# Optimization experiments

Measured on AMD Instinct MI355X. Metric: run time of the kernel, lower is better.

Reference implementation:

```python
import jax, jax.numpy as jnp
import numpy as np

B, M, L = 100, 100, 8
N = M * L
EPS = 1e-5  # torch BatchNorm2d default eps


def _conv(x, w, b, stride, pad):
    y = jax.lax.conv_general_dilated(x, w, (stride, stride), [(pad, pad), (pad, pad)],
                                     dimension_numbers=('NCHW', 'OIHW', 'NCHW'))
    return y + b[None, :, None, None]


def _convT(x, w, b, stride, pad):
    # torch ConvTranspose2d weight layout: (in_ch, out_ch, kH, kW)
    k = w.shape[2]
    wt = jnp.flip(w, (2, 3)).transpose(1, 0, 2, 3)  # -> OIHW
    p = k - 1 - pad
    y = jax.lax.conv_general_dilated(x, wt, (1, 1), [(p, p), (p, p)],
                                     lhs_dilation=(stride, stride),
                                     dimension_numbers=('NCHW', 'OIHW', 'NCHW'))
    return y + b[None, :, None, None]


def _bn(x):
    # BatchNorm2d constructed fresh in forward: weight=1, bias=0, batch stats (biased var)
    mean = x.mean(axis=(0, 2, 3), keepdims=True)
    var = x.var(axis=(0, 2, 3), keepdims=True)
    return (x - mean) / jnp.sqrt(var + EPS)


def _leaky(x):
    return jnp.where(x >= 0, x, 0.01 * x)


def _forward(x, conv1_w, conv1_b, conv2_w, conv2_b, conv3_w, conv3_b, conv4_w, conv4_b,
             fc_w, fc_b, dec_w, dec_b, ct1_w, ct1_b, ct2_w, ct2_b, ct3_w, ct3_b,
             ct4_w, ct4_b, ct5_w, ct5_b):
    # ---- encoder ----
    h = _bn(_leaky(_conv(x, conv1_w, conv1_b, 2, 1)))   # (B,128,32,32)
    h = _bn(_leaky(_conv(h, conv2_w, conv2_b, 2, 1)))   # (B,256,16,16)
    h = _bn(_leaky(_conv(h, conv3_w, conv3_b, 2, 1)))   # (B,1024,8,8)
    h = _bn(_leaky(_conv(h, conv4_w, conv4_b, 2, 1)))   # (B,1024,4,4)
    eig = jax.nn.relu(h.reshape(B, -1) @ fc_w + fc_b)   # (B, 800)
    # ---- latent_sample (training branch) ----
    sig = eig.reshape(B, M, L)
    row = jnp.sqrt(float(M * L)) * jnp.fft.ifft2(sig)          # complex (B,M,L)
    # original builds C via numpy/scipy per-sample -> detached; circulant[i,j] = c[(i-j) % n]
    row_flat = jax.lax.stop_gradient(row.real.reshape(B, N))
    i = jnp.arange(N)
    idx = (i[:, None] - i[None, :]) % N                        # (N,N) circulant gather
    C = row_flat[:, idx]                                       # (B,N,N)
    # original: Sigma_batch_eps[:, i] = eigenvalue (noise zeta is dead code), via numpy -> detached
    Y = jnp.fft.fft2(jax.lax.stop_gradient(sig)).real          # (B,M,L)
    # ---- decoder ----
    d = (Y.reshape(B, N) @ dec_w + dec_b).reshape(B, 1024, 3, 3)
    d = _convT(d, ct1_w, ct1_b, 2, 1)   # (B,512,5,5)
    d = _convT(d, ct2_w, ct2_b, 2, 0)   # (B,256,11,11)
    d = _convT(d, ct3_w, ct3_b, 2, 0)   # (B,128,23,23)
    d = _convT(d, ct4_w, ct4_b, 2, 0)   # (B,64,47,47)
    d = _convT(d, ct5_w, ct5_b, 1, 0)   # (B,1,49,49)
    return d, C, eig


def setup_inputs():
    key = jax.random.key(0)
    ks = jax.random.split(key, 16)

    def wv(k, shape, fan_in):
        return (jax.random.normal(k, shape, jnp.float32) / np.sqrt(fan_in)).astype(jnp.float32)

    return {
        'x': jax.random.normal(ks[0], (B, 1, 64, 64), jnp.float32),
        'conv1_w': wv(ks[1], (128, 1, 3, 3), 9), 'conv1_b': jnp.zeros((128,), jnp.float32),
        'conv2_w': wv(ks[2], (256, 128, 3, 3), 128 * 9), 'conv2_b': jnp.zeros((256,), jnp.float32),
        'conv3_w': wv(ks[3], (1024, 256, 3, 3), 256 * 9), 'conv3_b': jnp.zeros((1024,), jnp.float32),
        'conv4_w': wv(ks[4], (1024, 1024, 3, 3), 1024 * 9), 'conv4_b': jnp.zeros((1024,), jnp.float32),
        'fc_w': wv(ks[5], (1024 * 16, N), 1024 * 16), 'fc_b': jnp.zeros((N,), jnp.float32),
        'dec_w': wv(ks[6], (N, 1024 * 9), N), 'dec_b': jnp.zeros((1024 * 9,), jnp.float32),
        'ct1_w': wv(ks[7], (1024, 512, 3, 3), 1024 * 9), 'ct1_b': jnp.zeros((512,), jnp.float32),
        'ct2_w': wv(ks[8], (512, 256, 3, 3), 512 * 9), 'ct2_b': jnp.zeros((256,), jnp.float32),
        'ct3_w': wv(ks[9], (256, 128, 3, 3), 256 * 9), 'ct3_b': jnp.zeros((128,), jnp.float32),
        'ct4_w': wv(ks[10], (128, 64, 3, 3), 128 * 9), 'ct4_b': jnp.zeros((64,), jnp.float32),
        'ct5_w': wv(ks[11], (64, 1, 3, 3), 64 * 9), 'ct5_b': jnp.zeros((1,), jnp.float32),
    }


def reference(x, conv1_w, conv1_b, conv2_w, conv2_b, conv3_w, conv3_b, conv4_w, conv4_b,
              fc_w, fc_b, dec_w, dec_b, ct1_w, ct1_b, ct2_w, ct2_b, ct3_w, ct3_b,
              ct4_w, ct4_b, ct5_w, ct5_b):
    return _forward(x, conv1_w, conv1_b, conv2_w, conv2_b, conv3_w, conv3_b, conv4_w, conv4_b,
                    fc_w, fc_b, dec_w, dec_b, ct1_w, ct1_b, ct2_w, ct2_b, ct3_w, ct3_b,
                    ct4_w, ct4_b, ct5_w, ct5_b)
```

## Files before the change

kernel.cpp:

```cpp
#include <hip/hip_runtime.h>
#include <math.h>

typedef __attribute__((ext_vector_type(8))) short bf16x8;
typedef __attribute__((ext_vector_type(4))) float f32x4;
typedef unsigned short u16;

__device__ __forceinline__ u16 f2bf(float f) {
    unsigned u = __builtin_bit_cast(unsigned, f);
    u += 0x7FFFu + ((u >> 16) & 1u);
    return (u16)(u >> 16);
}
__device__ __forceinline__ float bf2f(u16 h) {
    unsigned u = ((unsigned)h) << 16;
    return __builtin_bit_cast(float, u);
}

__device__ __align__(64) unsigned g_zeros[16];

__device__ __forceinline__ void gll16(const u16* g, u16* l) {
    __builtin_amdgcn_global_load_lds(
        (const __attribute__((address_space(1))) unsigned*)g,
        (__attribute__((address_space(3))) unsigned*)l, 16, 0, 0);
}

template<int MODE, int OUT, int BM, int BN, int SWIZ, bool STATS, bool PF>
__global__ __launch_bounds__(256, 3)
void gemm(const u16* __restrict__ Abf, const u16* __restrict__ Bw,
          const float* __restrict__ bias, void* __restrict__ outv,
          float* __restrict__ stat,
          int M, int N, int K, int lgC,
          int IH, int IW, int OH, int OW, int zchunk)
{
    constexpr int ANSEG = BM / 64;
    constexpr int ACALLS = BM / 64;
    constexpr int BCALLS = BN / 64;
    constexpr int RM = BM / 32, RN = BN / 32;
    __shared__ __align__(16) u16 As[BM * 32];
    __shared__ __align__(16) u16 Bs[BN * 32];
    const int t = threadIdx.x;
    const int lane = t & 63, wave = t >> 6;
    const int lm = lane & 15, quad = lane >> 4;
    const int wm = wave & 1, wn = wave >> 1;
    int mt, nt, z;
    if (SWIZ == 1) {
        int mtN = (M + BM - 1) / BM;
        int id = blockIdx.x;
        nt = id & 7; int j = id >> 3;
        mt = j % mtN; z = j / mtN;
    } else { mt = blockIdx.x; nt = blockIdx.y; z = blockIdx.z; }
    const int k0 = z * zchunk, kend = k0 + zchunk;

    const int sl_row  = (wave << 4) + (lane >> 2);
    const int sl_koff = (lane & 3) * 8;

    const u16* bsrc[BCALLS]; int bmask[BCALLS];
    #pragma unroll
    for (int s = 0; s < BCALLS; s++) {
        int rg = nt * BN + s * 64 + sl_row;
        bool ok = rg < N;
        bsrc[s] = ok ? (Bw + (size_t)rg * K + sl_koff)
                     : ((const u16*)g_zeros + sl_koff);
        bmask[s] = ok ? ~0 : 0;
    }

    const u16* asrc[ACALLS]; int amask[ACALLS];
    if constexpr (MODE == 0) {
        #pragma unroll
        for (int s = 0; s < ACALLS; s++) {
            int rg = mt * BM + s * 64 + sl_row;
            bool ok = rg < M;
            asrc[s] = ok ? (Abf + (size_t)rg * K + sl_koff)
                         : ((const u16*)g_zeros + sl_koff);
            amask[s] = ok ? ~0 : 0;
        }
    }
    const int arow = (ANSEG == 2) ? (t >> 1) : (t >> 2);
    const int akb  = (ANSEG == 2) ? (t & 1) * 16 : (t & 3) * 8;
    const int a_gm = mt * BM + arow;
    const bool a_in = a_gm < M;
    int oy = 0, ox = 0, bimg = 0;
    const int Cmask = (1 << lgC) - 1;
    int ic_s = 0, tap_s = 0;
    bool aok = a_in;
    const u16* aptr = Abf;
    if constexpr (MODE == 1) {
        int ohw = OH * OW;
        int g = a_in ? a_gm : 0;
        bimg = g / ohw; int r = g - bimg * ohw;
        oy = r / OW; ox = r - (r / OW) * OW;
        int kk0 = k0 + akb;
        tap_s = kk0 >> lgC; ic_s = kk0 & Cmask;
        int ky = tap_s / 3, kx = tap_s - (tap_s / 3) * 3;
        int iy = oy * 2 - 1 + ky, ix = ox * 2 - 1 + kx;
        aok = a_in && (unsigned)iy < (unsigned)IH && (unsigned)ix < (unsigned)IW;
        aptr = Abf + ((((size_t)bimg * IH + iy) * IW + ix) << lgC);
    }
    auto ldA = [&](uint4 (&v)[ANSEG]) {
        #pragma unroll
        for (int s = 0; s < ANSEG; s++) {
            uint4 x4 = make_uint4(0, 0, 0, 0);
            if (aok) x4 = *(const uint4*)(aptr + ic_s + s * 8);
            v[s] = x4;
        }
        ic_s += 32;
        if (ic_s > Cmask) {
            ic_s -= Cmask + 1;
            tap_s++;
            int ky = tap_s / 3, kx = tap_s - (tap_s / 3) * 3;
            int iy = oy * 2 - 1 + ky, ix = ox * 2 - 1 + kx;
            aok = a_in && (unsigned)iy < (unsigned)IH && (unsigned)ix < (unsigned)IW;
            aptr = Abf + ((((size_t)bimg * IH + iy) * IW + ix) << lgC);
        }
    };

    f32x4 acc[RM][RN];
    #pragma unroll
    for (int i = 0; i < RM; i++)
        #pragma unroll
        for (int j = 0; j < RN; j++) acc[i][j] = (f32x4){0.f, 0.f, 0.f, 0.f};

    uint4 va[ANSEG];
    if (MODE == 1 && PF) ldA(va);
    for (int kb = k0; kb < kend; kb += 32) {
        if constexpr (MODE == 1) {
            if (!PF) ldA(va);
            #pragma unroll
            for (int s = 0; s < ANSEG; s++)
                *(uint4*)&As[(((akb >> 3) + s) * BM + arow) * 8] = va[s];
        } else {
            #pragma unroll
            for (int s = 0; s < ACALLS; s++)
                gll16(asrc[s] + (kb & amask[s]),
                      &As[(size_t)(s * 64 + (wave << 4)) * 32]);
        }
        #pragma unroll
        for (int s = 0; s < BCALLS; s++)
            gll16(bsrc[s] + (kb & bmask[s]),
                  &Bs[(size_t)(s * 64 + (wave << 4)) * 32]);
        __syncthreads();
        if (MODE == 1 && PF && kb + 32 < kend) ldA(va);
        bf16x8 af[RM], bfr[RN];
        #pragma unroll
        for (int i = 0; i < RM; i++) {
            if constexpr (MODE == 0)
                af[i] = *(const bf16x8*)&As[(wm * (BM / 2) + i * 16 + lm) * 32 + quad * 8];
            else
                af[i] = *(const bf16x8*)&As[(size_t)(quad * BM + wm * (BM / 2) + i * 16 + lm) * 8];
        }
        #pragma unroll
        for (int j = 0; j < RN; j++)
            bfr[j] = *(const bf16x8*)&Bs[(wn * (BN / 2) + j * 16 + lm) * 32 + quad * 8];
        #pragma unroll
        for (int i = 0; i < RM; i++)
            #pragma unroll
            for (int j = 0; j < RN; j++)
                acc[i][j] = __builtin_amdgcn_mfma_f32_16x16x32_bf16(af[i], bfr[j], acc[i][j], 0, 0, 0);
        __syncthreads();
    }

    const int n_base = nt * BN + wn * (BN / 2);
    const int m_base = mt * BM + wm * (BM / 2);
    int nj[RN]; float bvj[RN];
    #pragma unroll
    for (int j = 0; j < RN; j++) {
        nj[j] = n_base + j * 16 + lm;
        bvj[j] = 0.f;
        if (nj[j] < N && OUT != 4) {
            if (OUT == 0 || OUT == 5) bvj[j] = bias[nj[j]];
            else if (z == 0) bvj[j] = bias[nj[j]];
        }
    }
    if constexpr (OUT == 4) {
        float* op = (float*)outv;
        #pragma unroll
        for (int i = 0; i < RM; i++)
            #pragma unroll
            for (int r = 0; r < 4; r++) {
                int m = m_base + i * 16 + quad * 4 + r;
                if (m >= M) continue;
                #pragma unroll
                for (int j = 0; j < RN; j++)
                    if (nj[j] < N) atomicAdd(&op[(size_t)m * N + nj[j]], acc[i][j][r]);
            }
    } else if constexpr (OUT == 5) {
        u16* op = (u16*)outv;
        #pragma unroll
        for (int j = 0; j < RN; j++) {
            if (nj[j] >= N) continue;
            int c = nj[j] / 9, hw = nj[j] - c * 9;
            #pragma unroll
            for (int i = 0; i < RM; i++)
                #pragma unroll
                for (int r = 0; r < 4; r++) {
                    int m = m_base + i * 16 + quad * 4 + r;
                    if (m >= M) continue;
                    op[((size_t)m * 9 + hw) * 1024 + c] = f2bf(acc[i][j][r] + bvj[j]);
                }
        }
    } else if constexpr (OUT == 0) {
        int ohw = OH * OW;
        float sj[RN], qj[RN];
        #pragma unroll
        for (int j = 0; j < RN; j++) { sj[j] = 0.f; qj[j] = 0.f; }
        #pragma unroll
        for (int i = 0; i < RM; i++) {
            int m0 = m_base + i * 16 + quad * 4;
            if (m0 >= M) continue;
            int b = m0 / ohw, pix = m0 - b * ohw;
            #pragma unroll
            for (int j = 0; j < RN; j++) {
                if (nj[j] >= N) continue;
                #pragma unroll
                for (int r = 0; r < 4; r++) {
                    float val = acc[i][j][r] + bvj[j];
                    ((u16*)outv)[((size_t)b * ohw + pix + r) * N + nj[j]] = f2bf(val);
                    if (STATS) {
                        float lv = val >= 0.f ? val : 0.01f * val;
                        sj[j] += lv; qj[j] += lv * lv;
                    }
                }
            }
        }
        if constexpr (STATS) {
            #pragma unroll
            for (int j = 0; j < RN; j++) {
                float s = sj[j], q = qj[j];
                s += __shfl_down(s, 32); q += __shfl_down(q, 32);
                s += __shfl_down(s, 16); q += __shfl_down(q, 16);
                if (quad == 0 && nj[j] < N) {
                    atomicAdd(&stat[nj[j]], s);
                    atomicAdd(&stat[N + nj[j]], q);
                }
            }
        }
    } else {
        int ohw = OH * OW;
        #pragma unroll
        for (int i = 0; i < RM; i++) {
            int m0 = m_base + i * 16 + quad * 4;
            if (m0 >= M) continue;
            int b = m0 / ohw, pix = m0 - b * ohw;
            #pragma unroll
            for (int j = 0; j < RN; j++) {
                if (nj[j] >= N) continue;
                #pragma unroll
                for (int r = 0; r < 4; r++)
                    atomicAdd(&((float*)outv)[((size_t)b * ohw + pix + r) * N + nj[j]],
                              acc[i][j][r] + bvj[j]);
            }
        }
    }
}

template<int BM, int BN>
__global__ __launch_bounds__(256, 3)
void gemm_ct(const u16* __restrict__ Abf, const u16* __restrict__ Wb,
             const float* __restrict__ bias, u16* __restrict__ out,
             int N, int lgC, int IH, int IW, int OH, int OW,
             int4 Kc, int4 Mc, int4 Hc, int4 Wc, int4 Oc, int4 Dy, int4 Dx)
{
    constexpr int ANSEG = BM / 64;
    constexpr int BCALLS = BN / 64;
    constexpr int RM = BM / 32, RN = BN / 32;
    const int c = blockIdx.z;
    const int Ks[4] = {Kc.x, Kc.y, Kc.z, Kc.w};
    const int Ms[4] = {Mc.x, Mc.y, Mc.z, Mc.w};
    const int Hs[4] = {Hc.x, Hc.y, Hc.z, Hc.w};
    const int Wsz[4]= {Wc.x, Wc.y, Wc.z, Wc.w};
    const int Os[4] = {Oc.x, Oc.y, Oc.z, Oc.w};
    const int Dys[4]= {Dy.x, Dy.y, Dy.z, Dy.w};
    const int Dxs[4]= {Dx.x, Dx.y, Dx.z, Dx.w};
    const int K = Ks[c], M = Ms[c], OHc = Hs[c], OWc = Wsz[c];
    const int dyp = Dys[c], dxp = Dxs[c];
    const int mt = blockIdx.x, nt = blockIdx.y;
    if (mt * BM >= M) return;
    const u16* Bw = Wb + Os[c];

    __shared__ __align__(16) u16 As[BM * 32];
    __shared__ __align__(16) u16 Bs[BN * 32];
    const int t = threadIdx.x;
    const int lane = t & 63, wave = t >> 6;
    const int lm = lane & 15, quad = lane >> 4;
    const int wm = wave & 1, wn = wave >> 1;

    const int sl_row  = (wave << 4) + (lane >> 2);
    const int sl_koff = (lane & 3) * 8;
    const u16* bsrc[BCALLS];
    #pragma unroll
    for (int s = 0; s < BCALLS; s++) {
        int rg = nt * BN + s * 64 + sl_row;
        bsrc[s] = Bw + (size_t)rg * K + sl_koff;
    }

    const int arow = (ANSEG == 2) ? (t >> 1) : (t >> 2);
    const int akb  = (ANSEG == 2) ? (t & 1) * 16 : (t & 3) * 8;
    const int a_gm = mt * BM + arow;
    const bool a_in = a_gm < M;
    const int ohwc = OHc * OWc;
    int g = a_in ? a_gm : 0;
    int bimg = g / ohwc; int rr = g - bimg * ohwc;
    int oy = rr / OWc, ox = rr - (rr / OWc) * OWc;

    const int Cmask = (1 << lgC) - 1;
    int ic_s = akb & Cmask;
    int ti_s = 0;
    bool aok; const u16* aptr;
    {
        int sh = 8 * (ti_s & 3);
        int dy = (int)(signed char)((dyp >> sh) & 255);
        int dx = (int)(signed char)((dxp >> sh) & 255);
        int iy = oy + dy, ix = ox + dx;
        aok = a_in && (unsigned)iy < (unsigned)IH && (unsigned)ix < (unsigned)IW;
        aptr = Abf + ((((size_t)bimg * IH + iy) * IW + ix) << lgC);
    }
    auto ldA = [&](uint4 (&v)[ANSEG]) {
        #pragma unroll
        for (int s = 0; s < ANSEG; s++) {
            uint4 x4 = make_uint4(0, 0, 0, 0);
            if (aok) x4 = *(const uint4*)(aptr + ic_s + s * 8);
            v[s] = x4;
        }
        ic_s += 32;
        if (ic_s > Cmask) {
            ic_s -= Cmask + 1;
            ti_s++;
            int sh = 8 * (ti_s & 3);
            int dy = (int)(signed char)((dyp >> sh) & 255);
            int dx = (int)(signed char)((dxp >> sh) & 255);
            int iy = oy + dy, ix = ox + dx;
            aok = a_in && (unsigned)iy < (unsigned)IH && (unsigned)ix < (unsigned)IW;
            aptr = Abf + ((((size_t)bimg * IH + iy) * IW + ix) << lgC);
        }
    };

    f32x4 acc[RM][RN];
    #pragma unroll
    for (int i = 0; i < RM; i++)
        #pragma unroll
        for (int j = 0; j < RN; j++) acc[i][j] = (f32x4){0.f, 0.f, 0.f, 0.f};

    uint4 va[ANSEG];
    ldA(va);
    for (int kb = 0; kb < K; kb += 32) {
        #pragma unroll
        for (int s = 0; s < ANSEG; s++)
            *(uint4*)&As[(((akb >> 3) + s) * BM + arow) * 8] = va[s];
        #pragma unroll
        for (int s = 0; s < BCALLS; s++)
            gll16(bsrc[s] + kb, &Bs[(size_t)(s * 64 + (wave << 4)) * 32]);
        __syncthreads();
        if (kb + 32 < K) ldA(va);
        bf16x8 af[RM], bfr[RN];
        #pragma unroll
        for (int i = 0; i < RM; i++)
            af[i] = *(const bf16x8*)&As[(size_t)(quad * BM + wm * (BM / 2) + i * 16 + lm) * 8];
        #pragma unroll
        for (int j = 0; j < RN; j++)
            bfr[j] = *(const bf16x8*)&Bs[(wn * (BN / 2) + j * 16 + lm) * 32 + quad * 8];
        #pragma unroll
        for (int i = 0; i < RM; i++)
            #pragma unroll
            for (int j = 0; j < RN; j++)
                acc[i][j] = __builtin_amdgcn_mfma_f32_16x16x32_bf16(af[i], bfr[j], acc[i][j], 0, 0, 0);
        __syncthreads();
    }

    const int n_base = nt * BN + wn * (BN / 2);
    const int m_base = mt * BM + wm * (BM / 2);
    const int cy = c >> 1, cx = c & 1;
    const int OHW = OH * OW;
    int nj[RN]; float bvj[RN];
    #pragma unroll
    for (int j = 0; j < RN; j++) {
        nj[j] = n_base + j * 16 + lm;
        bvj[j] = (nj[j] < N) ? bias[nj[j]] : 0.f;
    }
    #pragma unroll
    for (int i = 0; i < RM; i++)
        #pragma unroll
        for (int r = 0; r < 4; r++) {
            int m = m_base + i * 16 + quad * 4 + r;
            if (m >= M) continue;
            int b = m / ohwc, r2 = m - b * ohwc;
            int oyc = r2 / OWc, oxc = r2 - (r2 / OWc) * OWc;
            size_t ad0 = ((size_t)b * OHW + (2 * oyc + cy) * OW + 2 * oxc + cx) * N;
            #pragma unroll
            for (int j = 0; j < RN; j++)
                if (nj[j] < N) out[ad0 + nj[j]] = f2bf(acc[i][j][r] + bvj[j]);
        }
}

__global__ __launch_bounds__(256)
void convw_prep(const float* __restrict__ src, u16* __restrict__ dst, int lgC) {
    __shared__ float tl[9216];
    int CIN = 1 << lgC;
    int n = CIN * 9;
    size_t base = (size_t)blockIdx.x * n;
    for (int i = threadIdx.x; i < n; i += 256) tl[i] = src[base + i];
    __syncthreads();
    for (int j = threadIdx.x; j < n; j += 256) {
        int tap = j >> lgC, ic = j & (CIN - 1);
        dst[base + j] = f2bf(tl[ic * 9 + tap]);
    }
}

__global__ __launch_bounds__(256)
void transpose_cvt(const float* __restrict__ in, u16* __restrict__ out, int R, int C) {
    __shared__ float tl[32][33];
    int c0 = blockIdx.x * 32, r0 = blockIdx.y * 32;
    int tx = threadIdx.x & 31, ty = threadIdx.x >> 5;
    #pragma unroll
    for (int l = 0; l < 4; l++)
        tl[ty + 8 * l][tx] = in[(size_t)(r0 + ty + 8 * l) * C + c0 + tx];
    __syncthreads();
    #pragma unroll
    for (int l = 0; l < 4; l++)
        out[(size_t)(c0 + ty + 8 * l) * R + r0 + tx] = f2bf(tl[tx][ty + 8 * l]);
}

__global__ __launch_bounds__(256)
void ctw_fused(const float* __restrict__ in, u16* __restrict__ outw,
               int CIN, int P, int4 Kc, int4 Oc) {
    __shared__ float tl[32][33];
    int c0 = blockIdx.x * 32, r0 = blockIdx.y * 32;
    int C = gridDim.x * 32;
    int tx = threadIdx.x & 31, ty = threadIdx.x >> 5;
    #pragma unroll
    for (int l = 0; l < 4; l++)
        tl[ty + 8 * l][tx] = in[(size_t)(r0 + ty + 8 * l) * C + c0 + tx];
    __syncthreads();
    const int Ks[4] = {Kc.x, Kc.y, Kc.z, Kc.w};
    const int Os[4] = {Oc.x, Oc.y, Oc.z, Oc.w};
    int ic = r0 + tx;
    #pragma unroll
    for (int l = 0; l < 4; l++) {
        int cc = c0 + ty + 8 * l;
        int oc = cc / 9, tap = cc - 9 * oc;
        int ky = tap / 3, kx = tap - 3 * (tap / 3);
        int cyc = (P + ky) & 1, cxc = (P + kx) & 1;
        int cls = cyc * 2 + cxc;
        int nkx = ((P ^ cxc) & 1) ? 1 : 2;
        int ti = (ky >> 1) * nkx + (kx >> 1);
        outw[Os[cls] + (size_t)oc * Ks[cls] + ti * CIN + ic] = f2bf(tl[tx][ty + 8 * l]);
    }
}

__global__ __launch_bounds__(256)
void fcw_prep(const float* __restrict__ in, u16* __restrict__ out) {
    __shared__ float tl[32][33];
    int n0 = blockIdx.x * 32, c0 = blockIdx.y * 32, hw = blockIdx.z;
    int tx = threadIdx.x & 31, ty = threadIdx.x >> 5;
    #pragma unroll
    for (int l = 0; l < 4; l++)
        tl[ty + 8 * l][tx] = in[((size_t)(c0 + ty + 8 * l) * 16 + hw) * 800 + n0 + tx];
    __syncthreads();
    #pragma unroll
    for (int l = 0; l < 4; l++)
        out[(size_t)(n0 + ty + 8 * l) * 16384 + hw * 1024 + c0 + tx] = f2bf(tl[tx][ty + 8 * l]);
}

__global__ __launch_bounds__(256)
void wt5_prep(const float* __restrict__ in, u16* __restrict__ out) {
    int idx = blockIdx.x * 256 + threadIdx.x;
    if (idx >= 576) return;
    int tap = idx >> 6, ic = idx & 63;
    out[idx] = f2bf(in[ic * 9 + tap]);
}

__global__ __launch_bounds__(256)
void conv1_nhwc(const float* __restrict__ x, const float* __restrict__ w,
                const float* __restrict__ bias, u16* __restrict__ out) {
    int idx = blockIdx.x * 256 + threadIdx.x;
    if (idx >= 100 * 1024 * 128) return;
    int oc = idx & 127;
    int pix = (idx >> 7) & 1023;
    int b = idx >> 17;
    int oy = pix >> 5, ox = pix & 31;
    int iy0 = oy * 2 - 1, ix0 = ox * 2 - 1;
    float acc = bias[oc];
    const float* ip = x + (size_t)b * 4096;
    const float* wp = w + oc * 9;
    #pragma unroll
    for (int ky = 0; ky < 3; ky++) {
        int iy = iy0 + ky;
        if ((unsigned)iy >= 64u) continue;
        #pragma unroll
        for (int kx = 0; kx < 3; kx++) {
            int ix = ix0 + kx;
            if ((unsigned)ix >= 64u) continue;
            acc = fmaf(ip[iy * 64 + ix], wp[ky * 3 + kx], acc);
        }
    }
    out[idx] = f2bf(acc);
}

__global__ __launch_bounds__(256)
void bnstat8(const u16* __restrict__ x, float* __restrict__ accum, int C, int total) {
    __shared__ float ls[2048];
    for (int i = threadIdx.x; i < 2 * C; i += 256) ls[i] = 0.f;
    __syncthreads();
    int base = (blockIdx.x * 256 + threadIdx.x) * 8;
    int stride = gridDim.x * 256 * 8;
    float s[8], q[8];
    #pragma unroll
    for (int r = 0; r < 8; r++) { s[r] = 0.f; q[r] = 0.f; }
    for (int i = base; i < total; i += stride) {
        uint4 v = *(const uint4*)(x + i);
        const unsigned* w = (const unsigned*)&v;
        #pragma unroll
        for (int h = 0; h < 4; h++) {
            float v0 = __builtin_bit_cast(float, w[h] << 16);
            float v1 = __builtin_bit_cast(float, w[h] & 0xFFFF0000u);
            v0 = v0 >= 0.f ? v0 : 0.01f * v0;
            v1 = v1 >= 0.f ? v1 : 0.01f * v1;
            s[2 * h] += v0;     q[2 * h] += v0 * v0;
            s[2 * h + 1] += v1; q[2 * h + 1] += v1 * v1;
        }
    }
    int c0 = base & (C - 1);
    #pragma unroll
    for (int r = 0; r < 8; r++) {
        atomicAdd(&ls[c0 + r], s[r]);
        atomicAdd(&ls[C + c0 + r], q[r]);
    }
    __syncthreads();
    for (int i = threadIdx.x; i < 2 * C; i += 256) atomicAdd(&accum[i], ls[i]);
}

__global__ __launch_bounds__(256)
void bnapply8(const u16* __restrict__ x, u16* __restrict__ out,
              const float* __restrict__ accum, int C, int total, float invcnt) {
    int i8 = (blockIdx.x * 256 + threadIdx.x) * 8;
    if (i8 >= total) return;
    int c0 = i8 & (C - 1);
    uint4 v = *(const uint4*)(x + i8);
    const unsigned* w = (const unsigned*)&v;
    uint4 o;
    unsigned* ow = (unsigned*)&o;
    #pragma unroll
    for (int h = 0; h < 4; h++) {
        float m0 = accum[c0 + 2 * h] * invcnt, m1 = accum[c0 + 2 * h + 1] * invcnt;
        float q0 = accum[C + c0 + 2 * h] * invcnt, q1 = accum[C + c0 + 2 * h + 1] * invcnt;
        float in0 = rsqrtf(q0 - m0 * m0 + 1e-5f);
        float in1 = rsqrtf(q1 - m1 * m1 + 1e-5f);
        float v0 = __builtin_bit_cast(float, w[h] << 16);
        float v1 = __builtin_bit_cast(float, w[h] & 0xFFFF0000u);
        v0 = v0 >= 0.f ? v0 : 0.01f * v0;
        v1 = v1 >= 0.f ? v1 : 0.01f * v1;
        unsigned r0 = f2bf((v0 - m0) * in0);
        unsigned r1 = f2bf((v1 - m1) * in1);
        ow[h] = r0 | (r1 << 16);
    }
    *(uint4*)(out + i8) = o;
}

__global__ __launch_bounds__(256)
void bnstat4f(const float* __restrict__ x, float* __restrict__ accum, int C, int total) {
    __shared__ float ls[2048];
    for (int i = threadIdx.x; i < 2 * C; i += 256) ls[i] = 0.f;
    __syncthreads();
    int base = (blockIdx.x * 256 + threadIdx.x) * 4;
    int stride = gridDim.x * 1024;
    float s[4] = {0, 0, 0, 0}, q[4] = {0, 0, 0, 0};
    for (int i = base; i < total; i += stride) {
        f32x4 v = *(const f32x4*)(x + i);
        #pragma unroll
        for (int r = 0; r < 4; r++) {
            float vv = v[r]; vv = vv >= 0.f ? vv : 0.01f * vv;
            s[r] += vv; q[r] += vv * vv;
        }
    }
    int c0 = base & (C - 1);
    #pragma unroll
    for (int r = 0; r < 4; r++) {
        atomicAdd(&ls[c0 + r], s[r]);
        atomicAdd(&ls[C + c0 + r], q[r]);
    }
    __syncthreads();
    for (int i = threadIdx.x; i < 2 * C; i += 256) atomicAdd(&accum[i], ls[i]);
}

__global__ __launch_bounds__(256)
void bnapply4f(const float* __restrict__ x, u16* __restrict__ out,
               const float* __restrict__ accum, int C, int total, float invcnt) {
    int i4 = (blockIdx.x * 256 + threadIdx.x) * 4;
    if (i4 >= total) return;
    int c0 = i4 & (C - 1);
    f32x4 v = *(const f32x4*)(x + i4);
    unsigned r4[4];
    #pragma unroll
    for (int r = 0; r < 4; r++) {
        float m = accum[c0 + r] * invcnt;
        float var = accum[C + c0 + r] * invcnt - m * m;
        float inv = rsqrtf(var + 1e-5f);
        float vv = v[r]; vv = vv >= 0.f ? vv : 0.01f * vv;
        r4[r] = f2bf((vv - m) * inv);
    }
    *(uint2*)(out + i4) = make_uint2(r4[0] | (r4[1] << 16), r4[2] | (r4[3] << 16));
}

__global__ __launch_bounds__(256)
void finalize_relu(const float* __restrict__ acc, const float* __restrict__ bias,
                   float* __restrict__ out) {
    int i = blockIdx.x * 256 + threadIdx.x;
    if (i >= 100 * 800) return;
    float v = acc[i] + bias[i % 800];
    out[i] = fmaxf(v, 0.f);
}

__global__ __launch_bounds__(256)
void dft_real(const float* __restrict__ eig, float* __restrict__ Yr, u16* __restrict__ Yrb) {
    __shared__ float se[800];
    __shared__ float ctab[800];
    int b = blockIdx.x;
    for (int i = threadIdx.x; i < 800; i += 256) {
        se[i] = eig[b * 800 + i];
        ctab[i] = cospif(i * 0.0025f);
    }
    __syncthreads();
    int o0 = blockIdx.y * 400;
    for (int oi = o0 + threadIdx.x; oi < o0 + 400; oi += 256) {
        int k1 = oi >> 3, k2 = oi & 7;
        int d1 = k1 * 8, d2 = k2 * 100;
        float acc0 = 0.f, acc1 = 0.f;
        int p1 = 0;
        for (int n1 = 0; n1 < 100; n1 += 2) {
            int p = p1;
            #pragma unroll
            for (int n2 = 0; n2 < 8; n2++) {
                acc0 = fmaf(se[n1 * 8 + n2], ctab[p], acc0);
                p += d2; if (p >= 800) p -= 800;
            }
            int pb = p1 + d1; if (pb >= 800) pb -= 800;
            int p2 = pb;
            #pragma unroll
            for (int n2 = 0; n2 < 8; n2++) {
                acc1 = fmaf(se[(n1 + 1) * 8 + n2], ctab[p2], acc1);
                p2 += d2; if (p2 >= 800) p2 -= 800;
            }
            p1 = pb + d1; if (p1 >= 800) p1 -= 800;
        }
        float acc = acc0 + acc1;
        Yr[b * 800 + oi] = acc;
        Yrb[b * 800 + oi] = f2bf(acc);
    }
}

__global__ __launch_bounds__(256)
void build_C4(const float* __restrict__ Yr, float* __restrict__ C) {
    int idx = blockIdx.x * 256 + threadIdx.x;
    if (idx >= 100 * 800 * 200) return;
    int j4 = (idx % 200) * 4; int tt = idx / 200;
    int i = tt % 800;         int b = tt / 800;
    const float* y = Yr + b * 800;
    f32x4 v;
    #pragma unroll
    for (int r = 0; r < 4; r++) {
        int k = i - (j4 + r);
        k += (k >> 31) & 800;
        v[r] = y[k] * 0.035355339059327376f;
    }
    ((f32x4*)C)[idx] = v;
}

__global__ __launch_bounds__(256)
void convT5(const u16* __restrict__ in, const u16* __restrict__ w,
            const float* __restrict__ bias, float* __restrict__ out) {
    int idx = blockIdx.x * 256 + threadIdx.x;
    if (idx >= 100 * 49 * 49) return;
    int ox = idx % 49; int t2 = idx / 49;
    int oy = t2 % 49;  int b = t2 / 49;
    float ac[8];
    #pragma unroll
    for (int r = 0; r < 8; r++) ac[r] = 0.f;
    for (int ky = 0; ky < 3; ky++) {
        int iy = oy - ky;
        if ((unsigned)iy >= 47u) continue;
        for (int kx = 0; kx < 3; kx++) {
            int ix = ox - kx;
            if ((unsigned)ix >= 47u) continue;
            const uint4* ip = (const uint4*)(in + (((size_t)b * 47 + iy) * 47 + ix) * 64);
            const uint4* wp = (const uint4*)(w + (ky * 3 + kx) * 64);
            #pragma unroll
            for (int g = 0; g < 8; g++) {
                uint4 av = ip[g], wv = wp[g];
                const unsigned* aa = (const unsigned*)&av;
                const unsigned* ww = (const unsigned*)&wv;
                #pragma unroll
                for (int h = 0; h < 4; h++) {
                    float a0 = __builtin_bit_cast(float, aa[h] << 16);
                    float a1 = __builtin_bit_cast(float, aa[h] & 0xFFFF0000u);
                    float w0 = __builtin_bit_cast(float, ww[h] << 16);
                    float w1 = __builtin_bit_cast(float, ww[h] & 0xFFFF0000u);
                    int rix = ((g & 1) << 2) | h;
                    ac[rix] = fmaf(a0, w0, ac[rix]);
                    ac[rix] = fmaf(a1, w1, ac[rix]);
                }
            }
        }
    }
    out[idx] = bias[0] + ((ac[0] + ac[1]) + (ac[2] + ac[3]))
                       + ((ac[4] + ac[5]) + (ac[6] + ac[7]));
}

struct CTClass { int T, OHc, OWc, dyp, dxp, off, K; };
static void ct_params(int P, int OH, int OW, int CIN, int OC, CTClass cls[4]) {
    int off = 0;
    for (int c = 0; c < 4; c++) {
        int cy = c >> 1, cx = c & 1;
        int kys[2], dys[2], nky = 0, kxs[2], dxs[2], nkx = 0;
        for (int ky = 0; ky < 3; ky++)
            if (((cy + P + ky) & 1) == 0) { kys[nky] = ky; dys[nky] = (cy + P - ky) / 2; nky++; }
        for (int kx = 0; kx < 3; kx++)
            if (((cx + P + kx) & 1) == 0) { kxs[nkx] = kx; dxs[nkx] = (cx + P - kx) / 2; nkx++; }
        CTClass& cc = cls[c];
        cc.T = nky * nkx;
        cc.OHc = (OH - cy + 1) >> 1; cc.OWc = (OW - cx + 1) >> 1;
        cc.dyp = 0; cc.dxp = 0;
        int ti = 0;
        for (int a = 0; a < nky; a++)
            for (int b2 = 0; b2 < nkx; b2++, ti++) {
                cc.dyp |= (dys[a] & 255) << (8 * ti);
                cc.dxp |= (dxs[b2] & 255) << (8 * ti);
            }
        cc.off = off; cc.K = CIN * cc.T;
        off += OC * cc.K;
    }
}

template<int BM, int BN>
static void launch_ct(hipStream_t s, const u16* in, const u16* W, const float* bias, u16* outp,
                      int lgC, int OC, int IH, int IW, int OH, int OW, const CTClass* cls) {
    int maxMT = 0;
    for (int c = 0; c < 4; c++) {
        int mt = (100 * cls[c].OHc * cls[c].OWc + BM - 1) / BM;
        if (mt > maxMT) maxMT = mt;
    }
    dim3 g(maxMT, OC / BN, 4);
    gemm_ct<BM, BN><<<g, 256, 0, s>>>(in, W, bias, outp, OC, lgC, IH, IW, OH, OW,
        make_int4(cls[0].K, cls[1].K, cls[2].K, cls[3].K),
        make_int4(100*cls[0].OHc*cls[0].OWc, 100*cls[1].OHc*cls[1].OWc,
                  100*cls[2].OHc*cls[2].OWc, 100*cls[3].OHc*cls[3].OWc),
        make_int4(cls[0].OHc, cls[1].OHc, cls[2].OHc, cls[3].OHc),
        make_int4(cls[0].OWc, cls[1].OWc, cls[2].OWc, cls[3].OWc),
        make_int4(cls[0].off, cls[1].off, cls[2].off, cls[3].off),
        make_int4(cls[0].dyp, cls[1].dyp, cls[2].dyp, cls[3].dyp),
        make_int4(cls[0].dxp, cls[1].dxp, cls[2].dxp, cls[3].dxp));
}

static void launch_ctw(hipStream_t s, const float* w, u16* outw,
                       int CIN, int OC, int P, const CTClass* cls) {
    dim3 g((OC * 9) / 32, CIN / 32);
    ctw_fused<<<g, 256, 0, s>>>(w, outw, CIN, P,
        make_int4(cls[0].K, cls[1].K, cls[2].K, cls[3].K),
        make_int4(cls[0].off, cls[1].off, cls[2].off, cls[3].off));
}

extern "C" void kernel_launch(void* const* d_in, const int* in_sizes, int n_in,
                              void* d_out, int out_size, void* d_ws, size_t ws_size,
                              hipStream_t stream) {
    const float* x    = (const float*)d_in[0];
    const float* c1w  = (const float*)d_in[1];  const float* c1b = (const float*)d_in[2];
    const float* c2w  = (const float*)d_in[3];  const float* c2b = (const float*)d_in[4];
    const float* c3w  = (const float*)d_in[5];  const float* c3b = (const float*)d_in[6];
    const float* c4w  = (const float*)d_in[7];  const float* c4b = (const float*)d_in[8];
    const float* fcw  = (const float*)d_in[9];  const float* fcb = (const float*)d_in[10];
    const float* decw = (const float*)d_in[11]; const float* decb = (const float*)d_in[12];
    const float* t1w  = (const float*)d_in[13]; const float* t1b = (const float*)d_in[14];
    const float* t2w  = (const float*)d_in[15]; const float* t2b = (const float*)d_in[16];
    const float* t3w  = (const float*)d_in[17]; const float* t3b = (const float*)d_in[18];
    const float* t4w  = (const float*)d_in[19]; const float* t4b = (const float*)d_in[20];
    const float* t5w  = (const float*)d_in[21]; const float* t5b = (const float*)d_in[22];

    float* out = (float*)d_out;
    float* d_final = out;
    float* Cmat    = out + 240100;
    float* eig     = out + 240100 + 64000000;

    float* ws = (float*)d_ws;
    u16*   h1    = (u16*)(ws);
    u16*   W_fc  = (u16*)(ws);
    u16*   h2    = (u16*)(ws + 6553600);
    u16*   h3    = (u16*)(ws + 9830400);
    u16*   W_c2  = (u16*)(ws + 13107200);
    u16*   W_c3  = (u16*)(ws + 13254656);
    u16*   W_c4  = (u16*)(ws + 14434304);
    float* h4f   = ws + 19152896;
    u16*   h4    = (u16*)(ws + 20791296);
    float* accs  = ws + 21610496;
    float* facc  = ws + 21618688;
    float* Yr    = ws + 21698688;
    u16*   Yrb   = (u16*)(ws + 21778688);
    u16*   d0    = (u16*)(ws + 21818688);
    u16*   W_dec = (u16*)(ws + 22279488);
    float* acc1 = accs, *acc2 = accs + 2048, *acc3 = accs + 4096, *acc4 = accs + 6144;
    u16*   W_t   = (u16*)(ws);
    u16*   o1    = (u16*)(ws + 4718592);
    u16*   o2    = (u16*)(ws + 5358592);
    u16*   o3    = (u16*)(ws + 6907392);
    u16*   o4    = (u16*)(ws + 10292992);
    u16*   W_t5  = (u16*)(ws + 17361792);

    #define GRID(n) dim3(((n) + 255) / 256)

    hipMemsetAsync(accs, 0, (8192 + 80000) * 4, stream);

    conv1_nhwc<<<GRID(13107200), 256, 0, stream>>>(x, c1w, c1b, h1);
    bnstat8<<<1024, 256, 0, stream>>>(h1, acc1, 128, 13107200);
    bnapply8<<<GRID(1638400), 256, 0, stream>>>(h1, h1, acc1, 128, 13107200, 1.f / 102400.f);

    convw_prep<<<dim3(256), 256, 0, stream>>>(c2w, W_c2, 7);
    gemm<1, 0, 128, 128, 0, true, false><<<dim3(200, 2, 1), 256, 0, stream>>>(
        h1, W_c2, c2b, h2, acc2, 25600, 256, 1152, 7, 32, 32, 16, 16, 1152);
    bnapply8<<<GRID(819200), 256, 0, stream>>>(h2, h2, acc2, 256, 6553600, 1.f / 25600.f);

    convw_prep<<<dim3(1024), 256, 0, stream>>>(c3w, W_c3, 8);
    gemm<1, 0, 128, 128, 1, true, false><<<dim3(400, 1, 1), 256, 0, stream>>>(
        h2, W_c3, c3b, h3, acc3, 6400, 1024, 2304, 8, 16, 16, 8, 8, 2304);
    bnapply8<<<GRID(819200), 256, 0, stream>>>(h3, h3, acc3, 1024, 6553600, 1.f / 6400.f);

    convw_prep<<<dim3(1024), 256, 0, stream>>>(c4w, W_c4, 10);
    hipMemsetAsync(h4f, 0, 1638400 * 4, stream);
    gemm<1, 1, 64, 128, 1, false, true><<<dim3(400, 1, 1), 256, 0, stream>>>(
        h3, W_c4, c4b, h4f, nullptr, 1600, 1024, 9216, 10, 8, 8, 4, 4, 4608);
    bnstat4f<<<1024, 256, 0, stream>>>(h4f, acc4, 1024, 1638400);
    bnapply4f<<<GRID(409600), 256, 0, stream>>>(h4f, h4, acc4, 1024, 1638400, 1.f / 1600.f);

    fcw_prep<<<dim3(25, 32, 16), 256, 0, stream>>>(fcw, W_fc);
    gemm<0, 4, 64, 64, 0, false, false><<<dim3(2, 13, 16), 256, 0, stream>>>(
        h4, W_fc, nullptr, facc, nullptr, 100, 800, 16384, 0, 0, 0, 0, 0, 1024);
    finalize_relu<<<GRID(80000), 256, 0, stream>>>(facc, fcb, eig);

    dft_real<<<dim3(100, 2), 256, 0, stream>>>(eig, Yr, Yrb);
    build_C4<<<GRID(16000000), 256, 0, stream>>>(Yr, Cmat);

    transpose_cvt<<<dim3(288, 25), 256, 0, stream>>>(decw, W_dec, 800, 9216);
    gemm<0, 5, 64, 64, 0, false, false><<<dim3(2, 144, 1), 256, 0, stream>>>(
        Yrb, W_dec, decb, d0, nullptr, 100, 9216, 800, 0, 0, 0, 0, 0, 800);

    CTClass c1c[4], c2c[4], c3c[4], c4c[4];
    ct_params(1, 5, 5, 1024, 512, c1c);
    ct_params(0, 11, 11, 512, 256, c2c);
    ct_params(0, 23, 23, 256, 128, c3c);
    ct_params(0, 47, 47, 128, 64, c4c);

    launch_ctw(stream, t1w, W_t, 1024, 512, 1, c1c);
    launch_ct<64, 64>(stream, d0, W_t, t1b, o1, 10, 512, 3, 3, 5, 5, c1c);

    launch_ctw(stream, t2w, W_t, 512, 256, 0, c2c);
    launch_ct<64, 128>(stream, o1, W_t, t2b, o2, 9, 256, 5, 5, 11, 11, c2c);

    launch_ctw(stream, t3w, W_t, 256, 128, 0, c3c);
    launch_ct<64, 128>(stream, o2, W_t, t3b, o3, 8, 128, 11, 11, 23, 23, c3c);

    launch_ctw(stream, t4w, W_t, 128, 64, 0, c4c);
    launch_ct<128, 64>(stream, o3, W_t, t4b, o4, 7, 64, 23, 23, 47, 47, c4c);

    wt5_prep<<<GRID(576), 256, 0, stream>>>(t5w, W_t5);
    convT5<<<GRID(240100), 256, 0, stream>>>(o4, W_t5, t5b, d_final);

    #undef GRID
}
```

Baseline: 1.134 ms.

## Load implicit-GEMM conv tiles via direct global-to-LDS with fragment-major layout

The im2col A-operand of the conv and transposed-conv GEMMs was loaded through registers, with an optional register prefetch, and then stored to LDS. It now uses global_load_lds direct copies with per-row pointers that advance along K, backed by a larger zero buffer for padded taps. LDS is re-laid out so each 16-row fragment stores its k-chunks contiguously, and the FC bias+ReLU kernel is fused into the DFT kernel to save a launch. The register prefetch overlap is dropped, and addressing now relies on the zero buffer being large enough for the channel offsets.

```diff
diff --git a/kernel.cpp b/kernel.cpp
--- a/kernel.cpp
+++ b/kernel.cpp
@@ -15,7 +15,7 @@
     return __builtin_bit_cast(float, u);
 }
 
-__device__ __align__(64) unsigned g_zeros[16];
+__device__ __align__(64) u16 g_zerow[4096];
 
 __device__ __forceinline__ void gll16(const u16* g, u16* l) {
     __builtin_amdgcn_global_load_lds(
@@ -23,7 +23,7 @@
         (__attribute__((address_space(3))) unsigned*)l, 16, 0, 0);
 }
 
-template<int MODE, int OUT, int BM, int BN, int SWIZ, bool STATS, bool PF>
+template<int MODE, int OUT, int BM, int BN, int SWIZ, bool STATS>
 __global__ __launch_bounds__(256, 3)
 void gemm(const u16* __restrict__ Abf, const u16* __restrict__ Bw,
           const float* __restrict__ bias, void* __restrict__ outv,
@@ -31,9 +31,7 @@
           int M, int N, int K, int lgC,
           int IH, int IW, int OH, int OW, int zchunk)
 {
-    constexpr int ANSEG = BM / 64;
-    constexpr int ACALLS = BM / 64;
-    constexpr int BCALLS = BN / 64;
+    constexpr int ACALLS = BM / 64, BCALLS = BN / 64;
     constexpr int RM = BM / 32, RN = BN / 32;
     __shared__ __align__(16) u16 As[BM * 32];
     __shared__ __align__(16) u16 Bs[BN * 32];
@@ -50,68 +48,48 @@
     } else { mt = blockIdx.x; nt = blockIdx.y; z = blockIdx.z; }
     const int k0 = z * zchunk, kend = k0 + zchunk;
 
-    const int sl_row  = (wave << 4) + (lane >> 2);
-    const int sl_koff = (lane & 3) * 8;
-
-    const u16* bsrc[BCALLS]; int bmask[BCALLS];
+    const int sr16  = lane & 15;
+    const int skoff = (lane >> 4) * 8;
+
+    const u16* bptr[BCALLS]; int bstep[BCALLS];
     #pragma unroll
     for (int s = 0; s < BCALLS; s++) {
-        int rg = nt * BN + s * 64 + sl_row;
+        int rg = nt * BN + s * 64 + (wave << 4) + sr16;
         bool ok = rg < N;
-        bsrc[s] = ok ? (Bw + (size_t)rg * K + sl_koff)
-                     : ((const u16*)g_zeros + sl_koff);
-        bmask[s] = ok ? ~0 : 0;
-    }
-
-    const u16* asrc[ACALLS]; int amask[ACALLS];
+        bptr[s] = ok ? (Bw + (size_t)rg * K + k0 + skoff) : (g_zerow + skoff);
+        bstep[s] = ok ? 32 : 0;
+    }
+
+    const u16* aptr[ACALLS]; int astep[ACALLS];
+    int p_b[ACALLS], p_oy[ACALLS], p_ox[ACALLS]; bool p_in[ACALLS];
+    const int CIN = 1 << lgC;
+    int ic_s = 0, tap_s = 0;
     if constexpr (MODE == 0) {
         #pragma unroll
         for (int s = 0; s < ACALLS; s++) {
-            int rg = mt * BM + s * 64 + sl_row;
+            int rg = mt * BM + s * 64 + (wave << 4) + sr16;
             bool ok = rg < M;
-            asrc[s] = ok ? (Abf + (size_t)rg * K + sl_koff)
-                         : ((const u16*)g_zeros + sl_koff);
-            amask[s] = ok ? ~0 : 0;
-        }
-    }
-    const int arow = (ANSEG == 2) ? (t >> 1) : (t >> 2);
-    const int akb  = (ANSEG == 2) ? (t & 1) * 16 : (t & 3) * 8;
-    const int a_gm = mt * BM + arow;
-    const bool a_in = a_gm < M;
-    int oy = 0, ox = 0, bimg = 0;
-    const int Cmask = (1 << lgC) - 1;
-    int ic_s = 0, tap_s = 0;
-    bool aok = a_in;
-    const u16* aptr = Abf;
-    if constexpr (MODE == 1) {
+            aptr[s] = ok ? (Abf + (size_t)rg * K + k0 + skoff) : (g_zerow + skoff);
+            astep[s] = ok ? 32 : 0;
+        }
+    } else {
         int ohw = OH * OW;
-        int g = a_in ? a_gm : 0;
-        bimg = g / ohw; int r = g - bimg * ohw;
-        oy = r / OW; ox = r - (r / OW) * OW;
-        int kk0 = k0 + akb;
-        tap_s = kk0 >> lgC; ic_s = kk0 & Cmask;
+        tap_s = k0 >> lgC; ic_s = k0 & (CIN - 1);
         int ky = tap_s / 3, kx = tap_s - (tap_s / 3) * 3;
-        int iy = oy * 2 - 1 + ky, ix = ox * 2 - 1 + kx;
-        aok = a_in && (unsigned)iy < (unsigned)IH && (unsigned)ix < (unsigned)IW;
-        aptr = Abf + ((((size_t)bimg * IH + iy) * IW + ix) << lgC);
-    }
-    auto ldA = [&](uint4 (&v)[ANSEG]) {
-        #pragma unroll
-        for (int s = 0; s < ANSEG; s++) {
-            uint4 x4 = make_uint4(0, 0, 0, 0);
-            if (aok) x4 = *(const uint4*)(aptr + ic_s + s * 8);
-            v[s] = x4;
-        }
-        ic_s += 32;
-        if (ic_s > Cmask) {
-            ic_s -= Cmask + 1;
-            tap_s++;
-            int ky = tap_s / 3, kx = tap_s - (tap_s / 3) * 3;
+        #pragma unroll
+        for (int s = 0; s < ACALLS; s++) {
+            int rg = mt * BM + s * 64 + (wave << 4) + sr16;
+            bool in = rg < M;
+            int g = in ? rg : 0;
+            int bb = g / ohw; int r = g - bb * ohw;
+            int oy = r / OW, ox = r - (r / OW) * OW;
+            p_in[s] = in; p_b[s] = bb; p_oy[s] = oy; p_ox[s] = ox;
             int iy = oy * 2 - 1 + ky, ix = ox * 2 - 1 + kx;
-            aok = a_in && (unsigned)iy < (unsigned)IH && (unsigned)ix < (unsigned)IW;
-            aptr = Abf + ((((size_t)bimg * IH + iy) * IW + ix) << lgC);
-        }
-    };
+            bool ok = in && (unsigned)iy < (unsigned)IH && (unsigned)ix < (unsigned)IW;
+            aptr[s] = ok ? (Abf + ((((size_t)bb * IH + iy) * IW + ix) << lgC) + ic_s + skoff)
+                         : (g_zerow + ic_s + skoff);
+        }
+    }
 
     f32x4 acc[RM][RN];
     #pragma unroll
@@ -119,37 +97,45 @@
         #pragma unroll
         for (int j = 0; j < RN; j++) acc[i][j] = (f32x4){0.f, 0.f, 0.f, 0.f};
 
-    uint4 va[ANSEG];
-    if (MODE == 1 && PF) ldA(va);
     for (int kb = k0; kb < kend; kb += 32) {
-        if constexpr (MODE == 1) {
-            if (!PF) ldA(va);
-            #pragma unroll
-            for (int s = 0; s < ANSEG; s++)
-                *(uint4*)&As[(((akb >> 3) + s) * BM + arow) * 8] = va[s];
+        #pragma unroll
+        for (int s = 0; s < ACALLS; s++)
+            gll16(aptr[s], &As[(size_t)(s * 64 + (wave << 4)) * 32]);
+        #pragma unroll
+        for (int s = 0; s < BCALLS; s++)
+            gll16(bptr[s], &Bs[(size_t)(s * 64 + (wave << 4)) * 32]);
+        #pragma unroll
+        for (int s = 0; s < BCALLS; s++) bptr[s] += bstep[s];
+        if constexpr (MODE == 0) {
+            #pragma unroll
+            for (int s = 0; s < ACALLS; s++) aptr[s] += astep[s];
         } else {
-            #pragma unroll
-            for (int s = 0; s < ACALLS; s++)
-                gll16(asrc[s] + (kb & amask[s]),
-                      &As[(size_t)(s * 64 + (wave << 4)) * 32]);
-        }
-        #pragma unroll
-        for (int s = 0; s < BCALLS; s++)
-            gll16(bsrc[s] + (kb & bmask[s]),
-                  &Bs[(size_t)(s * 64 + (wave << 4)) * 32]);
+            ic_s += 32;
+            if (ic_s >= CIN) {
+                ic_s = 0; tap_s++;
+                if (tap_s < 9) {
+                    int ky = tap_s / 3, kx = tap_s - (tap_s / 3) * 3;
+                    #pragma unroll
+                    for (int s = 0; s < ACALLS; s++) {
+                        int iy = p_oy[s] * 2 - 1 + ky, ix = p_ox[s] * 2 - 1 + kx;
+                        bool ok = p_in[s] && (unsigned)iy < (unsigned)IH && (unsigned)ix < (unsigned)IW;
+                        aptr[s] = ok ? (Abf + ((((size_t)p_b[s] * IH + iy) * IW + ix) << lgC) + skoff)
+                                     : (g_zerow + skoff);
+                    }
+                }
+            } else {
+                #pragma unroll
+                for (int s = 0; s < ACALLS; s++) aptr[s] += 32;
+            }
+        }
         __syncthreads();
-        if (MODE == 1 && PF && kb + 32 < kend) ldA(va);
         bf16x8 af[RM], bfr[RN];
         #pragma unroll
-        for (int i = 0; i < RM; i++) {
-            if constexpr (MODE == 0)
-                af[i] = *(const bf16x8*)&As[(wm * (BM / 2) + i * 16 + lm) * 32 + quad * 8];
-            else
-                af[i] = *(const bf16x8*)&As[(size_t)(quad * BM + wm * (BM / 2) + i * 16 + lm) * 8];
-        }
+        for (int i = 0; i < RM; i++)
+            af[i] = *(const bf16x8*)&As[((wm * (BM / 2) + i * 16) >> 4) * 512 + quad * 128 + lm * 8];
         #pragma unroll
         for (int j = 0; j < RN; j++)
-            bfr[j] = *(const bf16x8*)&Bs[(wn * (BN / 2) + j * 16 + lm) * 32 + quad * 8];
+            bfr[j] = *(const bf16x8*)&Bs[((wn * (BN / 2) + j * 16) >> 4) * 512 + quad * 128 + lm * 8];
         #pragma unroll
         for (int i = 0; i < RM; i++)
             #pragma unroll
@@ -259,8 +245,7 @@
              int N, int lgC, int IH, int IW, int OH, int OW,
              int4 Kc, int4 Mc, int4 Hc, int4 Wc, int4 Oc, int4 Dy, int4 Dx)
 {
-    constexpr int ANSEG = BM / 64;
-    constexpr int BCALLS = BN / 64;
+    constexpr int ACALLS = BM / 64, BCALLS = BN / 64;
     constexpr int RM = BM / 32, RN = BN / 32;
     const int c = blockIdx.z;
     const int Ks[4] = {Kc.x, Kc.y, Kc.z, Kc.w};
@@ -283,80 +268,79 @@
     const int lm = lane & 15, quad = lane >> 4;
     const int wm = wave & 1, wn = wave >> 1;
 
-    const int sl_row  = (wave << 4) + (lane >> 2);
-    const int sl_koff = (lane & 3) * 8;
-    const u16* bsrc[BCALLS];
+    const int sr16  = lane & 15;
+    const int skoff = (lane >> 4) * 8;
+
+    const u16* bptr[BCALLS];
     #pragma unroll
     for (int s = 0; s < BCALLS; s++) {
-        int rg = nt * BN + s * 64 + sl_row;
-        bsrc[s] = Bw + (size_t)rg * K + sl_koff;
-    }
-
-    const int arow = (ANSEG == 2) ? (t >> 1) : (t >> 2);
-    const int akb  = (ANSEG == 2) ? (t & 1) * 16 : (t & 3) * 8;
-    const int a_gm = mt * BM + arow;
-    const bool a_in = a_gm < M;
+        int rg = nt * BN + s * 64 + (wave << 4) + sr16;
+        bptr[s] = Bw + (size_t)rg * K + skoff;
+    }
+
     const int ohwc = OHc * OWc;
-    int g = a_in ? a_gm : 0;
-    int bimg = g / ohwc; int rr = g - bimg * ohwc;
-    int oy = rr / OWc, ox = rr - (rr / OWc) * OWc;
-
-    const int Cmask = (1 << lgC) - 1;
-    int ic_s = akb & Cmask;
-    int ti_s = 0;
-    bool aok; const u16* aptr;
+    const int CIN = 1 << lgC;
+    int p_b[ACALLS], p_oy[ACALLS], p_ox[ACALLS]; bool p_in[ACALLS];
+    const u16* aptr[ACALLS];
+    int ic_s = 0, ti_s = 0;
     {
-        int sh = 8 * (ti_s & 3);
-        int dy = (int)(signed char)((dyp >> sh) & 255);
-        int dx = (int)(signed char)((dxp >> sh) & 255);
-        int iy = oy + dy, ix = ox + dx;
-        aok = a_in && (unsigned)iy < (unsigned)IH && (unsigned)ix < (unsigned)IW;
-        aptr = Abf + ((((size_t)bimg * IH + iy) * IW + ix) << lgC);
-    }
-    auto ldA = [&](uint4 (&v)[ANSEG]) {
-        #pragma unroll
-        for (int s = 0; s < ANSEG; s++) {
-            uint4 x4 = make_uint4(0, 0, 0, 0);
-            if (aok) x4 = *(const uint4*)(aptr + ic_s + s * 8);
-            v[s] = x4;
-        }
+        int dy = (int)(signed char)(dyp & 255);
+        int dx = (int)(signed char)(dxp & 255);
+        #pragma unroll
+        for (int s = 0; s < ACALLS; s++) {
+            int rg = mt * BM + s * 64 + (wave << 4) + sr16;
+            bool in = rg < M;
+            int g = in ? rg : 0;
+            int bb = g / ohwc; int rr = g - bb * ohwc;
+            int oy = rr / OWc, ox = rr - (rr / OWc) * OWc;
+            p_in[s] = in; p_b[s] = bb; p_oy[s] = oy; p_ox[s] = ox;
+            int iy = oy + dy, ix = ox + dx;
+            bool ok = in && (unsigned)iy < (unsigned)IH && (unsigned)ix < (unsigned)IW;
+            aptr[s] = ok ? (Abf + ((((size_t)bb * IH + iy) * IW + ix) << lgC) + skoff)
+                         : (g_zerow + skoff);
+        }
+    }
+
+    f32x4 acc[RM][RN];
+    #pragma unroll
+    for (int i = 0; i < RM; i++)
+        #pragma unroll
+        for (int j = 0; j < RN; j++) acc[i][j] = (f32x4){0.f, 0.f, 0.f, 0.f};
+
+    for (int kb = 0; kb < K; kb += 32) {
+        #pragma unroll
+        for (int s = 0; s < ACALLS; s++)
+            gll16(aptr[s], &As[(size_t)(s * 64 + (wave << 4)) * 32]);
+        #pragma unroll
+        for (int s = 0; s < BCALLS; s++)
+            gll16(bptr[s], &Bs[(size_t)(s * 64 + (wave << 4)) * 32]);
+        #pragma unroll
+        for (int s = 0; s < BCALLS; s++) bptr[s] += 32;
         ic_s += 32;
-        if (ic_s > Cmask) {
-            ic_s -= Cmask + 1;
-            ti_s++;
+        if (ic_s >= CIN) {
+            ic_s = 0; ti_s++;
             int sh = 8 * (ti_s & 3);
             int dy = (int)(signed char)((dyp >> sh) & 255);
             int dx = (int)(signed char)((dxp >> sh) & 255);
-            int iy = oy + dy, ix = ox + dx;
-            aok = a_in && (unsigned)iy < (unsigned)IH && (unsigned)ix < (unsigned)IW;
-            aptr = Abf + ((((size_t)bimg * IH + iy) * IW + ix) << lgC);
-        }
-    };
-
-    f32x4 acc[RM][RN];
-    #pragma unroll
-    for (int i = 0; i < RM; i++)
-        #pragma unroll
-        for (int j = 0; j < RN; j++) acc[i][j] = (f32x4){0.f, 0.f, 0.f, 0.f};
-
-    uint4 va[ANSEG];
-    ldA(va);
-    for (int kb = 0; kb < K; kb += 32) {
-        #pragma unroll
-        for (int s = 0; s < ANSEG; s++)
-            *(uint4*)&As[(((akb >> 3) + s) * BM + arow) * 8] = va[s];
-        #pragma unroll
-        for (int s = 0; s < BCALLS; s++)
-            gll16(bsrc[s] + kb, &Bs[(size_t)(s * 64 + (wave << 4)) * 32]);
+            #pragma unroll
+            for (int s = 0; s < ACALLS; s++) {
+                int iy = p_oy[s] + dy, ix = p_ox[s] + dx;
+                bool ok = p_in[s] && (unsigned)iy < (unsigned)IH && (unsigned)ix < (unsigned)IW;
+                aptr[s] = ok ? (Abf + ((((size_t)p_b[s] * IH + iy) * IW + ix) << lgC) + skoff)
+                             : (g_zerow + skoff);
+            }
+        } else {
+            #pragma unroll
+            for (int s = 0; s < ACALLS; s++) aptr[s] += 32;
+        }
         __syncthreads();
-        if (kb + 32 < K) ldA(va);
         bf16x8 af[RM], bfr[RN];
         #pragma unroll
         for (int i = 0; i < RM; i++)
-            af[i] = *(const bf16x8*)&As[(size_t)(quad * BM + wm * (BM / 2) + i * 16 + lm) * 8];
+            af[i] = *(const bf16x8*)&As[((wm * (BM / 2) + i * 16) >> 4) * 512 + quad * 128 + lm * 8];
         #pragma unroll
         for (int j = 0; j < RN; j++)
-            bfr[j] = *(const bf16x8*)&Bs[(wn * (BN / 2) + j * 16 + lm) * 32 + quad * 8];
+            bfr[j] = *(const bf16x8*)&Bs[((wn * (BN / 2) + j * 16) >> 4) * 512 + quad * 128 + lm * 8];
         #pragma unroll
         for (int i = 0; i < RM; i++)
             #pragma unroll
@@ -600,21 +584,15 @@
 }
 
 __global__ __launch_bounds__(256)
-void finalize_relu(const float* __restrict__ acc, const float* __restrict__ bias,
-                   float* __restrict__ out) {
-    int i = blockIdx.x * 256 + threadIdx.x;
-    if (i >= 100 * 800) return;
-    float v = acc[i] + bias[i % 800];
-    out[i] = fmaxf(v, 0.f);
-}
-
-__global__ __launch_bounds__(256)
-void dft_real(const float* __restrict__ eig, float* __restrict__ Yr, u16* __restrict__ Yrb) {
+void dft_real(const float* __restrict__ facc, const float* __restrict__ fcb,
+              float* __restrict__ eig, float* __restrict__ Yr, u16* __restrict__ Yrb) {
     __shared__ float se[800];
     __shared__ float ctab[800];
     int b = blockIdx.x;
     for (int i = threadIdx.x; i < 800; i += 256) {
-        se[i] = eig[b * 800 + i];
+        float v = fmaxf(facc[b * 800 + i] + fcb[i], 0.f);
+        se[i] = v;
+        if (blockIdx.y == 0) eig[b * 800 + i] = v;
         ctab[i] = cospif(i * 0.0025f);
     }
     __syncthreads();
@@ -810,32 +788,31 @@
     bnapply8<<<GRID(1638400), 256, 0, stream>>>(h1, h1, acc1, 128, 13107200, 1.f / 102400.f);
 
     convw_prep<<<dim3(256), 256, 0, stream>>>(c2w, W_c2, 7);
-    gemm<1, 0, 128, 128, 0, true, false><<<dim3(200, 2, 1), 256, 0, stream>>>(
+    gemm<1, 0, 128, 128, 0, true><<<dim3(200, 2, 1), 256, 0, stream>>>(
         h1, W_c2, c2b, h2, acc2, 25600, 256, 1152, 7, 32, 32, 16, 16, 1152);
     bnapply8<<<GRID(819200), 256, 0, stream>>>(h2, h2, acc2, 256, 6553600, 1.f / 25600.f);
 
     convw_prep<<<dim3(1024), 256, 0, stream>>>(c3w, W_c3, 8);
-    gemm<1, 0, 128, 128, 1, true, false><<<dim3(400, 1, 1), 256, 0, stream>>>(
+    gemm<1, 0, 128, 128, 1, true><<<dim3(400, 1, 1), 256, 0, stream>>>(
         h2, W_c3, c3b, h3, acc3, 6400, 1024, 2304, 8, 16, 16, 8, 8, 2304);
     bnapply8<<<GRID(819200), 256, 0, stream>>>(h3, h3, acc3, 1024, 6553600, 1.f / 6400.f);
 
     convw_prep<<<dim3(1024), 256, 0, stream>>>(c4w, W_c4, 10);
     hipMemsetAsync(h4f, 0, 1638400 * 4, stream);
-    gemm<1, 1, 64, 128, 1, false, true><<<dim3(400, 1, 1), 256, 0, stream>>>(
+    gemm<1, 1, 64, 128, 1, false><<<dim3(400, 1, 1), 256, 0, stream>>>(
         h3, W_c4, c4b, h4f, nullptr, 1600, 1024, 9216, 10, 8, 8, 4, 4, 4608);
     bnstat4f<<<1024, 256, 0, stream>>>(h4f, acc4, 1024, 1638400);
     bnapply4f<<<GRID(409600), 256, 0, stream>>>(h4f, h4, acc4, 1024, 1638400, 1.f / 1600.f);
 
     fcw_prep<<<dim3(25, 32, 16), 256, 0, stream>>>(fcw, W_fc);
-    gemm<0, 4, 64, 64, 0, false, false><<<dim3(2, 13, 16), 256, 0, stream>>>(
+    gemm<0, 4, 64, 64, 0, false><<<dim3(2, 13, 16), 256, 0, stream>>>(
         h4, W_fc, nullptr, facc, nullptr, 100, 800, 16384, 0, 0, 0, 0, 0, 1024);
-    finalize_relu<<<GRID(80000), 256, 0, stream>>>(facc, fcb, eig);
-
-    dft_real<<<dim3(100, 2), 256, 0, stream>>>(eig, Yr, Yrb);
+
+    dft_real<<<dim3(100, 2), 256, 0, stream>>>(facc, fcb, eig, Yr, Yrb);
     build_C4<<<GRID(16000000), 256, 0, stream>>>(Yr, Cmat);
 
     transpose_cvt<<<dim3(288, 25), 256, 0, stream>>>(decw, W_dec, 800, 9216);
-    gemm<0, 5, 64, 64, 0, false, false><<<dim3(2, 144, 1), 256, 0, stream>>>(
+    gemm<0, 5, 64, 64, 0, false><<<dim3(2, 144, 1), 256, 0, stream>>>(
         Yrb, W_dec, decb, d0, nullptr, 100, 9216, 800, 0, 0, 0, 0, 0, 800);
 
     CTClass c1c[4], c2c[4], c3c[4], c4c[4];
```

Result: slower. 1.192 ms (+5.1%).
